# Kernel optimization log

Hardware: AMD Instinct MI355X
Metric: run time of the kernel (lower is better)

The kernel has to match this reference:

```python
import jax, jax.numpy as jnp
import numpy as np

B = 256      # number of drug pairs in the batch
N_PER = 40   # atoms per graph (equal-sized segments)
H = 128      # hidden_dim


def setup_inputs() -> dict:
    key = jax.random.key(0)
    k1, k2, kw1, kb1, kw2, kb2 = jax.random.split(key, 6)
    N = B * N_PER
    h1_atoms = jax.random.normal(k1, (N, H), dtype=jnp.float32)
    h2_atoms = jax.random.normal(k2, (N, H), dtype=jnp.float32)
    # sorted, equal-sized batch assignments (40 atoms per graph)
    batch1 = jnp.repeat(jnp.arange(B, dtype=jnp.int32), N_PER)
    batch2 = jnp.repeat(jnp.arange(B, dtype=jnp.int32), N_PER)
    s1 = 1.0 / np.sqrt(2 * H)
    s2 = 1.0 / np.sqrt(H)
    W1 = jax.random.uniform(kw1, (2 * H, H), jnp.float32, -s1, s1)
    b1 = jax.random.uniform(kb1, (H,), jnp.float32, -s1, s1)
    W2 = jax.random.uniform(kw2, (H, 1), jnp.float32, -s2, s2)
    b2 = jax.random.uniform(kb2, (1,), jnp.float32, -s2, s2)
    return {"h1_atoms": h1_atoms, "h2_atoms": h2_atoms, "batch1": batch1,
            "batch2": batch2, "W1": W1, "b1": b1, "W2": W2, "b2": b2}


def reference(h1_atoms, h2_atoms, batch1, batch2, W1, b1, W2, b2):
    # Equal-sized sorted segments -> reshape into [B, n, H] blocks.
    a1 = h1_atoms.reshape(B, N_PER, H)
    a2 = h2_atoms.reshape(B, N_PER, H)
    # cat([a1_exp, a2_exp], -1) @ W1  ==  a1 @ W1[:H] + a2 @ W1[H:]
    # (avoids materializing the [B,n1,n2,2H] concat)
    p1 = jnp.einsum('bid,dh->bih', a1, W1[:H])          # [B,n1,H]
    p2 = jnp.einsum('bjd,dh->bjh', a2, W1[H:])          # [B,n2,H]
    hidden = jnp.tanh(p1[:, :, None, :] + p2[:, None, :, :] + b1)  # [B,n1,n2,H]
    logits = jnp.einsum('bijh,h->bij', hidden, W2[:, 0]) + b2[0]   # [B,n1,n2]
    # global softmax over the flattened n1*n2 pair scores of each drug pair
    p = jax.nn.softmax(logits.reshape(B, -1), axis=-1).reshape(B, N_PER, N_PER)
    attn1 = p.sum(axis=2).reshape(-1)   # [num_atoms1]
    attn2 = p.sum(axis=1).reshape(-1)   # [num_atoms2]
    return attn1, attn2
```

## Files before the change

kernel.cpp:

```cpp
#include <hip/hip_runtime.h>

#define BB 256
#define NP 40
#define HH 128
#define EST 132
#define SST 44
#define NT 1024
#define AROWB 272
#define NROWP 48

typedef __attribute__((ext_vector_type(8))) short bf16x8;
typedef __attribute__((ext_vector_type(4))) float f32x4;

static __device__ __forceinline__ unsigned short f2bf(float f) {
    unsigned u = __float_as_uint(f);
    return (unsigned short)((u + 0x7FFFu + ((u >> 16) & 1u)) >> 16);
}

#define BATCH2(acc, ex0, ex1, ey0, ey1, ww0, ww1) do {            \
    float d0_ = fmaf((ex0), (ey0), 1.f);                          \
    float d1_ = fmaf((ex1), (ey1), 1.f);                          \
    float r_  = __builtin_amdgcn_rcpf(d0_ * d1_);                 \
    float n_  = fmaf((ww1), d0_, (ww0) * d1_);                    \
    acc = fmaf(n_, r_, acc);                                      \
} while (0)

__global__ __launch_bounds__(NT, 4) void ddi_fused(
    const float* __restrict__ h1, const float* __restrict__ h2,
    const float* __restrict__ W1, const float* __restrict__ b1,
    const float* __restrict__ W2, const float* __restrict__ b2,
    float* __restrict__ out)
{
    const int b = blockIdx.x;
    const int t = threadIdx.x;
    const int l = t & 63;
    const int w = t >> 6;

    __shared__ __align__(16) char  sAB[2*NROWP*AROWB];
    __shared__ __align__(16) float sE[2*NP*EST];
    __shared__ __align__(16) float sSE[NP*SST];
    __shared__ __align__(16) float sW2[HH];
    __shared__ float sRed[NT/64];
    __shared__ float sCL;

    const float L2E = 1.44269504088896340736f;
    const float K   = 2.88539008177792681472f;

    const int m  = w >> 3;
    const int hm = w & 7;
    const int hbase = hm*16 + ((l >> 4) << 2);
    const float* Wb = W1 + (size_t)m*HH*HH + hm*16 + (l & 15);
    float wraw[4][8];
    #pragma unroll
    for (int ks = 0; ks < 4; ++ks)
        #pragma unroll
        for (int j = 0; j < 8; ++j)
            wraw[ks][j] = Wb[(size_t)(ks*32 + ((l>>4)<<3) + j) * HH];
    float4 kbK = make_float4(0.f,0.f,0.f,0.f);
    if (m == 0) {
        float4 bv = *(const float4*)(b1 + hbase);
        kbK = make_float4(K*bv.x, K*bv.y, K*bv.z, K*bv.w);
    }

    #pragma unroll
    for (int pass = 0; pass < 2; ++pass) {
        int s = t + pass*NT;
        if (s < 2*NP*16) {
            int ms  = (s >= NP*16) ? 1 : 0;
            int rem = s - ms*NP*16;
            int r   = rem >> 4;
            int kg  = rem & 15;
            const float* src = (ms ? h2 : h1) + ((size_t)b*NP + r)*HH + kg*8;
            float4 v0 = *(const float4*)src;
            float4 v1 = *(const float4*)(src + 4);
            unsigned p0 = f2bf(v0.x) | ((unsigned)f2bf(v0.y) << 16);
            unsigned p1 = f2bf(v0.z) | ((unsigned)f2bf(v0.w) << 16);
            unsigned p2 = f2bf(v1.x) | ((unsigned)f2bf(v1.y) << 16);
            unsigned p3 = f2bf(v1.z) | ((unsigned)f2bf(v1.w) << 16);
            *(uint4*)(sAB + (ms*NROWP + r)*AROWB + kg*16) = make_uint4(p0,p1,p2,p3);
        }
    }
    if (t < HH) sW2[t] = W2[t];
    if (t < 64) {
        float c = W2[t] + W2[t + 64];
        #pragma unroll
        for (int off = 32; off > 0; off >>= 1) c += __shfl_down(c, off, 64);
        if (t == 0) sCL = (c + b2[0]) * L2E;
    }

    bf16x8 wf[4];
    #pragma unroll
    for (int ks = 0; ks < 4; ++ks) {
        #pragma unroll
        for (int j = 0; j < 8; ++j)
            ((unsigned short*)&wf[ks])[j] = f2bf(wraw[ks][j]);
    }
    __syncthreads();

    {
        const char* Ab = sAB + (m*NROWP + (l & 15))*AROWB + ((l >> 4) << 4);
        #pragma unroll
        for (int rn = 0; rn < 3; ++rn) {
            f32x4 c = {0.f, 0.f, 0.f, 0.f};
            #pragma unroll
            for (int ks = 0; ks < 4; ++ks) {
                bf16x8 af = *(const bf16x8*)(Ab + rn*(16*AROWB) + ks*64);
                c = __builtin_amdgcn_mfma_f32_16x16x32_bf16(wf[ks], af, c, 0, 0, 0);
            }
            int r = rn*16 + (l & 15);
            if (r < NP) {
                float4 ev;
                ev.x = __builtin_amdgcn_exp2f(fmaf(K, c[0], kbK.x));
                ev.y = __builtin_amdgcn_exp2f(fmaf(K, c[1], kbK.y));
                ev.z = __builtin_amdgcn_exp2f(fmaf(K, c[2], kbK.z));
                ev.w = __builtin_amdgcn_exp2f(fmaf(K, c[3], kbK.w));
                *(float4*)(sE + (m*NP + r)*EST + hbase) = ev;
            }
        }
    }
    __syncthreads();

    float lsum = 0.f;
    if (t < 800) {
        const int tile = t >> 2;
        const int hseg = t & 3;
        const int it = tile / 20;
        const int jt = tile - it * 20;
        const int h0 = hseg << 5;
        const float* e1b = sE + it*EST + h0;
        const float* e2b = sE + (NP + jt)*EST + h0;
        const float* wpb = sW2 + h0;
        float a[8];
        #pragma unroll
        for (int q = 0; q < 8; ++q) a[q] = 0.f;
        #pragma unroll
        for (int s = 0; s < 32; s += 4) {
            float4 wv = *(const float4*)(wpb + s);
            float4 e1v[4], e2v[2];
            #pragma unroll
            for (int rn = 0; rn < 4; ++rn) e1v[rn] = *(const float4*)(e1b + rn*10*EST + s);
            #pragma unroll
            for (int cn = 0; cn < 2; ++cn) e2v[cn] = *(const float4*)(e2b + cn*20*EST + s);
            #pragma unroll
            for (int rn = 0; rn < 4; ++rn)
                #pragma unroll
                for (int cn = 0; cn < 2; ++cn) {
                    BATCH2(a[rn*2+cn], e1v[rn].x, e1v[rn].y, e2v[cn].x, e2v[cn].y, wv.x, wv.y);
                    BATCH2(a[rn*2+cn], e1v[rn].z, e1v[rn].w, e2v[cn].z, e2v[cn].w, wv.z, wv.w);
                }
        }
        #pragma unroll
        for (int q = 0; q < 8; ++q) {
            a[q] += __shfl_xor(a[q], 1);
            a[q] += __shfl_xor(a[q], 2);
        }
        float s0 = (hseg==0) ? a[0] : (hseg==1) ? a[2] : (hseg==2) ? a[4] : a[6];
        float s1 = (hseg==0) ? a[1] : (hseg==1) ? a[3] : (hseg==2) ? a[5] : a[7];
        const float CL = sCL;
        const int row = it + 10*hseg;
        float pu0 = __builtin_amdgcn_exp2f(fmaf(s0, -K, CL));
        float pu1 = __builtin_amdgcn_exp2f(fmaf(s1, -K, CL));
        sSE[row*SST + jt]      = pu0;
        sSE[row*SST + jt + 20] = pu1;
        lsum = pu0 + pu1;
    }

    #pragma unroll
    for (int off = 32; off > 0; off >>= 1) lsum += __shfl_down(lsum, off, 64);
    if ((t & 63) == 0) sRed[t >> 6] = lsum;
    __syncthreads();
    float Z = 0.f;
    #pragma unroll
    for (int wv = 0; wv < NT/64; ++wv) Z += sRed[wv];
    const float rZ = __builtin_amdgcn_rcpf(Z);

    if (t < 320) {
        const int row = t >> 3, seg = t & 7;
        const float* p = sSE + row*SST + seg*5;
        float s = p[0] + p[1] + p[2] + p[3] + p[4];
        s += __shfl_down(s, 4, 8);
        s += __shfl_down(s, 2, 8);
        s += __shfl_down(s, 1, 8);
        if (seg == 0) out[b*NP + row] = s * rZ;
    } else if (t < 640) {
        const int q = t - 320;
        const int col = q >> 3, seg = q & 7;
        float s = 0.f;
        #pragma unroll
        for (int k = 0; k < 5; ++k) s += sSE[(seg*5 + k)*SST + col];
        s += __shfl_down(s, 4, 8);
        s += __shfl_down(s, 2, 8);
        s += __shfl_down(s, 1, 8);
        if (seg == 0) out[BB*NP + b*NP + col] = s * rZ;
    }
}

extern "C" void kernel_launch(void* const* d_in, const int* in_sizes, int n_in,
                              void* d_out, int out_size, void* d_ws, size_t ws_size,
                              hipStream_t stream) {
    const float* h1 = (const float*)d_in[0];
    const float* h2 = (const float*)d_in[1];
    const float* W1 = (const float*)d_in[4];
    const float* b1 = (const float*)d_in[5];
    const float* W2 = (const float*)d_in[6];
    const float* b2 = (const float*)d_in[7];
    float* out = (float*)d_out;

    hipLaunchKernelGGL(ddi_fused, dim3(BB), dim3(NT), 0, stream,
                       h1, h2, W1, b1, W2, b2, out);
}
```

Measured before the change: 17.48 us.

## Load atom rows straight into MFMA fragments with register double-buffering

Removes the shared-memory staging of bf16 atom features. Each lane now loads its own A-fragment rows from global memory, converts them to bf16 in registers and runs the MFMA directly, using two register buffers so the next row tile's load overlaps the current tile's compute and epilogue. This drops a __syncthreads and the LDS writes and reads, but each row is now loaded redundantly by all 8 hm waves instead of once. Register pressure also rises, and the launch_bounds occupancy hint of 4 is removed.

```diff
diff --git a/kernel.cpp b/kernel.cpp
--- a/kernel.cpp
+++ b/kernel.cpp
@@ -1,4 +1,5 @@
 #include <hip/hip_runtime.h>
+#include <hip/hip_bf16.h>
 
 #define BB 256
 #define NP 40
@@ -6,15 +7,14 @@
 #define EST 132
 #define SST 44
 #define NT 1024
-#define AROWB 272
-#define NROWP 48
 
 typedef __attribute__((ext_vector_type(8))) short bf16x8;
 typedef __attribute__((ext_vector_type(4))) float f32x4;
 
-static __device__ __forceinline__ unsigned short f2bf(float f) {
-    unsigned u = __float_as_uint(f);
-    return (unsigned short)((u + 0x7FFFu + ((u >> 16) & 1u)) >> 16);
+static __device__ __forceinline__ short bfs(float f) {
+    union { __hip_bfloat16 h; short s; } u;
+    u.h = __float2bfloat16(f);
+    return u.s;
 }
 
 #define BATCH2(acc, ex0, ex1, ey0, ey1, ww0, ww1) do {            \
@@ -25,7 +25,45 @@
     acc = fmaf(n_, r_, acc);                                      \
 } while (0)
 
-__global__ __launch_bounds__(NT, 4) void ddi_fused(
+#define LOADA(buf, rn) do {                                        \
+    int r_  = (rn)*16 + lr;                                        \
+    int rc_ = (r_ < NP) ? r_ : NP-1;    \
+    const float* s_ = Am + ((size_t)b*NP + rc_)*HH + (l4<<3);      \
+    _Pragma("unroll")                                              \
+    for (int ks_ = 0; ks_ < 4; ++ks_) {                            \
+        buf[2*ks_]   = *(const float4*)(s_ + ks_*32);              \
+        buf[2*ks_+1] = *(const float4*)(s_ + ks_*32 + 4);          \
+    }                                                              \
+} while (0)
+
+#define COMPUTE(buf, cacc) do {                                    \
+    bf16x8 af_[4];                                                 \
+    _Pragma("unroll")                                              \
+    for (int ks_ = 0; ks_ < 4; ++ks_) {                            \
+        short* ap_ = (short*)&af_[ks_];                            \
+        ap_[0]=bfs(buf[2*ks_].x);   ap_[1]=bfs(buf[2*ks_].y);      \
+        ap_[2]=bfs(buf[2*ks_].z);   ap_[3]=bfs(buf[2*ks_].w);      \
+        ap_[4]=bfs(buf[2*ks_+1].x); ap_[5]=bfs(buf[2*ks_+1].y);    \
+        ap_[6]=bfs(buf[2*ks_+1].z); ap_[7]=bfs(buf[2*ks_+1].w);    \
+    }                                                              \
+    _Pragma("unroll")                                              \
+    for (int ks_ = 0; ks_ < 4; ++ks_)                              \
+        cacc = __builtin_amdgcn_mfma_f32_16x16x32_bf16(wf[ks_], af_[ks_], cacc, 0, 0, 0); \
+} while (0)
+
+#define EPILOG(cacc, rn) do {                                      \
+    int r_ = (rn)*16 + lr;                                         \
+    if (r_ < NP) {                                                 \
+        float4 ev_;                                                \
+        ev_.x = __builtin_amdgcn_exp2f(fmaf(K, cacc[0], kbK.x));   \
+        ev_.y = __builtin_amdgcn_exp2f(fmaf(K, cacc[1], kbK.y));   \
+        ev_.z = __builtin_amdgcn_exp2f(fmaf(K, cacc[2], kbK.z));   \
+        ev_.w = __builtin_amdgcn_exp2f(fmaf(K, cacc[3], kbK.w));   \
+        *(float4*)(sE + (m*NP + r_)*EST + hbase) = ev_;            \
+    }                                                              \
+} while (0)
+
+__global__ __launch_bounds__(NT) void ddi_fused(
     const float* __restrict__ h1, const float* __restrict__ h2,
     const float* __restrict__ W1, const float* __restrict__ b1,
     const float* __restrict__ W2, const float* __restrict__ b2,
@@ -36,7 +74,6 @@
     const int l = t & 63;
     const int w = t >> 6;
 
-    __shared__ __align__(16) char  sAB[2*NROWP*AROWB];
     __shared__ __align__(16) float sE[2*NP*EST];
     __shared__ __align__(16) float sSE[NP*SST];
     __shared__ __align__(16) float sW2[HH];
@@ -48,38 +85,27 @@
 
     const int m  = w >> 3;
     const int hm = w & 7;
-    const int hbase = hm*16 + ((l >> 4) << 2);
-    const float* Wb = W1 + (size_t)m*HH*HH + hm*16 + (l & 15);
+    const int l4 = l >> 4;
+    const int lr = l & 15;
+    const int hbase = hm*16 + l4*4;
+    const float* Am = m ? h2 : h1;
+
+    const float* Wb = W1 + (size_t)m*HH*HH + hm*16 + lr;
     float wraw[4][8];
     #pragma unroll
     for (int ks = 0; ks < 4; ++ks)
         #pragma unroll
         for (int j = 0; j < 8; ++j)
-            wraw[ks][j] = Wb[(size_t)(ks*32 + ((l>>4)<<3) + j) * HH];
+            wraw[ks][j] = Wb[(size_t)(ks*32 + (l4<<3) + j) * HH];
+
+    float4 aA[8], aB[8];
+    LOADA(aA, 0);
+
     float4 kbK = make_float4(0.f,0.f,0.f,0.f);
     if (m == 0) {
         float4 bv = *(const float4*)(b1 + hbase);
         kbK = make_float4(K*bv.x, K*bv.y, K*bv.z, K*bv.w);
     }
-
-    #pragma unroll
-    for (int pass = 0; pass < 2; ++pass) {
-        int s = t + pass*NT;
-        if (s < 2*NP*16) {
-            int ms  = (s >= NP*16) ? 1 : 0;
-            int rem = s - ms*NP*16;
-            int r   = rem >> 4;
-            int kg  = rem & 15;
-            const float* src = (ms ? h2 : h1) + ((size_t)b*NP + r)*HH + kg*8;
-            float4 v0 = *(const float4*)src;
-            float4 v1 = *(const float4*)(src + 4);
-            unsigned p0 = f2bf(v0.x) | ((unsigned)f2bf(v0.y) << 16);
-            unsigned p1 = f2bf(v0.z) | ((unsigned)f2bf(v0.w) << 16);
-            unsigned p2 = f2bf(v1.x) | ((unsigned)f2bf(v1.y) << 16);
-            unsigned p3 = f2bf(v1.z) | ((unsigned)f2bf(v1.w) << 16);
-            *(uint4*)(sAB + (ms*NROWP + r)*AROWB + kg*16) = make_uint4(p0,p1,p2,p3);
-        }
-    }
     if (t < HH) sW2[t] = W2[t];
     if (t < 64) {
         float c = W2[t] + W2[t + 64];
@@ -91,33 +117,21 @@
     bf16x8 wf[4];
     #pragma unroll
     for (int ks = 0; ks < 4; ++ks) {
-        #pragma unroll
-        for (int j = 0; j < 8; ++j)
-            ((unsigned short*)&wf[ks])[j] = f2bf(wraw[ks][j]);
-    }
-    __syncthreads();
-
-    {
-        const char* Ab = sAB + (m*NROWP + (l & 15))*AROWB + ((l >> 4) << 4);
-        #pragma unroll
-        for (int rn = 0; rn < 3; ++rn) {
-            f32x4 c = {0.f, 0.f, 0.f, 0.f};
-            #pragma unroll
-            for (int ks = 0; ks < 4; ++ks) {
-                bf16x8 af = *(const bf16x8*)(Ab + rn*(16*AROWB) + ks*64);
-                c = __builtin_amdgcn_mfma_f32_16x16x32_bf16(wf[ks], af, c, 0, 0, 0);
-            }
-            int r = rn*16 + (l & 15);
-            if (r < NP) {
-                float4 ev;
-                ev.x = __builtin_amdgcn_exp2f(fmaf(K, c[0], kbK.x));
-                ev.y = __builtin_amdgcn_exp2f(fmaf(K, c[1], kbK.y));
-                ev.z = __builtin_amdgcn_exp2f(fmaf(K, c[2], kbK.z));
-                ev.w = __builtin_amdgcn_exp2f(fmaf(K, c[3], kbK.w));
-                *(float4*)(sE + (m*NP + r)*EST + hbase) = ev;
-            }
-        }
-    }
+        short* wp = (short*)&wf[ks];
+        #pragma unroll
+        for (int j = 0; j < 8; ++j) wp[j] = bfs(wraw[ks][j]);
+    }
+
+    f32x4 c0 = {0.f,0.f,0.f,0.f}, c1 = c0, c2 = c0;
+    COMPUTE(aA, c0);
+    LOADA(aB, 1);
+    EPILOG(c0, 0);
+    COMPUTE(aB, c1);
+    LOADA(aA, 2);
+    EPILOG(c1, 1);
+    COMPUTE(aA, c2);
+    EPILOG(c2, 2);
+
     __syncthreads();
 
     float lsum = 0.f;
```

Measured after the change: 24.73 us. +41.4%, slower.

## Split each drug pair across two half-row blocks with a second normalization kernel

Applied to the files above, without the earlier changes.

Each drug pair is now handled by two 512-thread blocks, each covering 20 of the 40 rows of the first graph. Partial softmax sums and row/column sums go to a workspace, and a small second kernel combines them and normalizes. The aim is to double the grid size and shrink each block for better occupancy and load balance across CUs. In exchange, each block recomputes the full h2 projection (redundant MFMA work), an extra kernel launch is added, and results make a round trip through global memory.

```diff
diff --git a/kernel.cpp b/kernel.cpp
--- a/kernel.cpp
+++ b/kernel.cpp
@@ -1,20 +1,22 @@
 #include <hip/hip_runtime.h>
+#include <hip/hip_bf16.h>
 
 #define BB 256
 #define NP 40
 #define HH 128
 #define EST 132
 #define SST 44
-#define NT 1024
+#define NT1 512
 #define AROWB 272
-#define NROWP 48
+#define WSPP 128
 
 typedef __attribute__((ext_vector_type(8))) short bf16x8;
 typedef __attribute__((ext_vector_type(4))) float f32x4;
 
-static __device__ __forceinline__ unsigned short f2bf(float f) {
-    unsigned u = __float_as_uint(f);
-    return (unsigned short)((u + 0x7FFFu + ((u >> 16) & 1u)) >> 16);
+static __device__ __forceinline__ short bfs(float f) {
+    union { __hip_bfloat16 h; short s; } u;
+    u.h = __float2bfloat16(f);
+    return u.s;
 }
 
 #define BATCH2(acc, ex0, ex1, ey0, ey1, ww0, ww1) do {            \
@@ -25,59 +27,57 @@
     acc = fmaf(n_, r_, acc);                                      \
 } while (0)
 
-__global__ __launch_bounds__(NT, 4) void ddi_fused(
+__global__ __launch_bounds__(NT1, 4) void ddi_k1(
     const float* __restrict__ h1, const float* __restrict__ h2,
     const float* __restrict__ W1, const float* __restrict__ b1,
     const float* __restrict__ W2, const float* __restrict__ b2,
-    float* __restrict__ out)
+    float* __restrict__ ws)
 {
-    const int b = blockIdx.x;
+    const int b    = blockIdx.x >> 1;
+    const int half = blockIdx.x & 1;
     const int t = threadIdx.x;
     const int l = t & 63;
     const int w = t >> 6;
-
-    __shared__ __align__(16) char  sAB[2*NROWP*AROWB];
-    __shared__ __align__(16) float sE[2*NP*EST];
-    __shared__ __align__(16) float sSE[NP*SST];
+    const int l4 = l >> 4;
+    const int lr = l & 15;
+    const int hm = w;
+    const int hbase = hm*16 + l4*4;
+
+    __shared__ __align__(16) char  sAB[60*AROWB];
+    __shared__ __align__(16) float sE[60*EST];
+    __shared__ __align__(16) float sSE[20*SST];
     __shared__ __align__(16) float sW2[HH];
-    __shared__ float sRed[NT/64];
+    __shared__ float sRed[8];
     __shared__ float sCL;
 
     const float L2E = 1.44269504088896340736f;
     const float K   = 2.88539008177792681472f;
 
-    const int m  = w >> 3;
-    const int hm = w & 7;
-    const int hbase = hm*16 + ((l >> 4) << 2);
-    const float* Wb = W1 + (size_t)m*HH*HH + hm*16 + (l & 15);
+    const float* Wb0 = W1 + hm*16 + lr;
+    const float* Wb1 = W1 + (size_t)HH*HH + hm*16 + lr;
     float wraw[4][8];
     #pragma unroll
     for (int ks = 0; ks < 4; ++ks)
         #pragma unroll
         for (int j = 0; j < 8; ++j)
-            wraw[ks][j] = Wb[(size_t)(ks*32 + ((l>>4)<<3) + j) * HH];
-    float4 kbK = make_float4(0.f,0.f,0.f,0.f);
-    if (m == 0) {
-        float4 bv = *(const float4*)(b1 + hbase);
-        kbK = make_float4(K*bv.x, K*bv.y, K*bv.z, K*bv.w);
-    }
+            wraw[ks][j] = Wb0[(size_t)(ks*32 + (l4<<3) + j) * HH];
 
     #pragma unroll
     for (int pass = 0; pass < 2; ++pass) {
-        int s = t + pass*NT;
-        if (s < 2*NP*16) {
-            int ms  = (s >= NP*16) ? 1 : 0;
-            int rem = s - ms*NP*16;
-            int r   = rem >> 4;
-            int kg  = rem & 15;
-            const float* src = (ms ? h2 : h1) + ((size_t)b*NP + r)*HH + kg*8;
+        int s = t + pass*NT1;
+        if (s < 60*16) {
+            int r  = s >> 4;
+            int kg = s & 15;
+            const float* src = (r < 20)
+                ? h1 + ((size_t)b*NP + half*20 + r)*HH + kg*8
+                : h2 + ((size_t)b*NP + (r-20))*HH + kg*8;
             float4 v0 = *(const float4*)src;
             float4 v1 = *(const float4*)(src + 4);
-            unsigned p0 = f2bf(v0.x) | ((unsigned)f2bf(v0.y) << 16);
-            unsigned p1 = f2bf(v0.z) | ((unsigned)f2bf(v0.w) << 16);
-            unsigned p2 = f2bf(v1.x) | ((unsigned)f2bf(v1.y) << 16);
-            unsigned p3 = f2bf(v1.z) | ((unsigned)f2bf(v1.w) << 16);
-            *(uint4*)(sAB + (ms*NROWP + r)*AROWB + kg*16) = make_uint4(p0,p1,p2,p3);
+            unsigned p0 = (unsigned short)bfs(v0.x) | ((unsigned)(unsigned short)bfs(v0.y) << 16);
+            unsigned p1 = (unsigned short)bfs(v0.z) | ((unsigned)(unsigned short)bfs(v0.w) << 16);
+            unsigned p2 = (unsigned short)bfs(v1.x) | ((unsigned)(unsigned short)bfs(v1.y) << 16);
+            unsigned p3 = (unsigned short)bfs(v1.z) | ((unsigned)(unsigned short)bfs(v1.w) << 16);
+            *(uint4*)(sAB + r*AROWB + kg*16) = make_uint4(p0,p1,p2,p3);
         }
     }
     if (t < HH) sW2[t] = W2[t];
@@ -88,47 +88,82 @@
         if (t == 0) sCL = (c + b2[0]) * L2E;
     }
 
-    bf16x8 wf[4];
+    bf16x8 wf0[4], wf1[4];
     #pragma unroll
     for (int ks = 0; ks < 4; ++ks) {
+        short* wp = (short*)&wf0[ks];
+        #pragma unroll
+        for (int j = 0; j < 8; ++j) wp[j] = bfs(wraw[ks][j]);
+    }
+    #pragma unroll
+    for (int ks = 0; ks < 4; ++ks)
         #pragma unroll
         for (int j = 0; j < 8; ++j)
-            ((unsigned short*)&wf[ks])[j] = f2bf(wraw[ks][j]);
+            wraw[ks][j] = Wb1[(size_t)(ks*32 + (l4<<3) + j) * HH];
+    #pragma unroll
+    for (int ks = 0; ks < 4; ++ks) {
+        short* wp = (short*)&wf1[ks];
+        #pragma unroll
+        for (int j = 0; j < 8; ++j) wp[j] = bfs(wraw[ks][j]);
+    }
+    float4 kbK;
+    {
+        float4 bv = *(const float4*)(b1 + hbase);
+        kbK = make_float4(K*bv.x, K*bv.y, K*bv.z, K*bv.w);
     }
     __syncthreads();
 
-    {
-        const char* Ab = sAB + (m*NROWP + (l & 15))*AROWB + ((l >> 4) << 4);
-        #pragma unroll
-        for (int rn = 0; rn < 3; ++rn) {
-            f32x4 c = {0.f, 0.f, 0.f, 0.f};
-            #pragma unroll
-            for (int ks = 0; ks < 4; ++ks) {
-                bf16x8 af = *(const bf16x8*)(Ab + rn*(16*AROWB) + ks*64);
-                c = __builtin_amdgcn_mfma_f32_16x16x32_bf16(wf[ks], af, c, 0, 0, 0);
-            }
-            int r = rn*16 + (l & 15);
-            if (r < NP) {
-                float4 ev;
-                ev.x = __builtin_amdgcn_exp2f(fmaf(K, c[0], kbK.x));
-                ev.y = __builtin_amdgcn_exp2f(fmaf(K, c[1], kbK.y));
-                ev.z = __builtin_amdgcn_exp2f(fmaf(K, c[2], kbK.z));
-                ev.w = __builtin_amdgcn_exp2f(fmaf(K, c[3], kbK.w));
-                *(float4*)(sE + (m*NP + r)*EST + hbase) = ev;
-            }
+    #pragma unroll
+    for (int rn = 0; rn < 2; ++rn) {
+        int rr = rn*16 + lr;
+        int rowc = (rr < 20) ? rr : 19;
+        const char* Ab = sAB + rowc*AROWB + (l4 << 4);
+        f32x4 c = {0.f,0.f,0.f,0.f};
+        #pragma unroll
+        for (int ks = 0; ks < 4; ++ks) {
+            bf16x8 af = *(const bf16x8*)(Ab + ks*64);
+            c = __builtin_amdgcn_mfma_f32_16x16x32_bf16(wf0[ks], af, c, 0, 0, 0);
+        }
+        if (rr < 20) {
+            float4 ev;
+            ev.x = __builtin_amdgcn_exp2f(fmaf(K, c[0], kbK.x));
+            ev.y = __builtin_amdgcn_exp2f(fmaf(K, c[1], kbK.y));
+            ev.z = __builtin_amdgcn_exp2f(fmaf(K, c[2], kbK.z));
+            ev.w = __builtin_amdgcn_exp2f(fmaf(K, c[3], kbK.w));
+            *(float4*)(sE + rr*EST + hbase) = ev;
+        }
+    }
+    #pragma unroll
+    for (int rn = 0; rn < 3; ++rn) {
+        int rr = rn*16 + lr;
+        int rowc = (rr < 40) ? rr : 39;
+        const char* Ab = sAB + (20 + rowc)*AROWB + (l4 << 4);
+        f32x4 c = {0.f,0.f,0.f,0.f};
+        #pragma unroll
+        for (int ks = 0; ks < 4; ++ks) {
+            bf16x8 af = *(const bf16x8*)(Ab + ks*64);
+            c = __builtin_amdgcn_mfma_f32_16x16x32_bf16(wf1[ks], af, c, 0, 0, 0);
+        }
+        if (rr < 40) {
+            float4 ev;
+            ev.x = __builtin_amdgcn_exp2f(K * c[0]);
+            ev.y = __builtin_amdgcn_exp2f(K * c[1]);
+            ev.z = __builtin_amdgcn_exp2f(K * c[2]);
+            ev.w = __builtin_amdgcn_exp2f(K * c[3]);
+            *(float4*)(sE + (20 + rr)*EST + hbase) = ev;
         }
     }
     __syncthreads();
 
     float lsum = 0.f;
-    if (t < 800) {
+    if (t < 400) {
         const int tile = t >> 2;
         const int hseg = t & 3;
         const int it = tile / 20;
-        const int jt = tile - it * 20;
+        const int jt = tile - it*20;
         const int h0 = hseg << 5;
         const float* e1b = sE + it*EST + h0;
-        const float* e2b = sE + (NP + jt)*EST + h0;
+        const float* e2b = sE + (20 + jt)*EST + h0;
         const float* wpb = sW2 + h0;
         float a[8];
         #pragma unroll
@@ -138,7 +173,7 @@
             float4 wv = *(const float4*)(wpb + s);
             float4 e1v[4], e2v[2];
             #pragma unroll
-            for (int rn = 0; rn < 4; ++rn) e1v[rn] = *(const float4*)(e1b + rn*10*EST + s);
+            for (int rn = 0; rn < 4; ++rn) e1v[rn] = *(const float4*)(e1b + rn*5*EST + s);
             #pragma unroll
             for (int cn = 0; cn < 2; ++cn) e2v[cn] = *(const float4*)(e2b + cn*20*EST + s);
             #pragma unroll
@@ -157,7 +192,7 @@
         float s0 = (hseg==0) ? a[0] : (hseg==1) ? a[2] : (hseg==2) ? a[4] : a[6];
         float s1 = (hseg==0) ? a[1] : (hseg==1) ? a[3] : (hseg==2) ? a[5] : a[7];
         const float CL = sCL;
-        const int row = it + 10*hseg;
+        const int row = it + 5*hseg;
         float pu0 = __builtin_amdgcn_exp2f(fmaf(s0, -K, CL));
         float pu1 = __builtin_amdgcn_exp2f(fmaf(s1, -K, CL));
         sSE[row*SST + jt]      = pu0;
@@ -171,27 +206,42 @@
     __syncthreads();
     float Z = 0.f;
     #pragma unroll
-    for (int wv = 0; wv < NT/64; ++wv) Z += sRed[wv];
-    const float rZ = __builtin_amdgcn_rcpf(Z);
-
-    if (t < 320) {
+    for (int wv = 0; wv < 8; ++wv) Z += sRed[wv];
+
+    float* wsp = ws + (size_t)b*WSPP + half*64;
+    if (t == 0) wsp[0] = Z;
+    if (t < 160) {
         const int row = t >> 3, seg = t & 7;
         const float* p = sSE + row*SST + seg*5;
         float s = p[0] + p[1] + p[2] + p[3] + p[4];
         s += __shfl_down(s, 4, 8);
         s += __shfl_down(s, 2, 8);
         s += __shfl_down(s, 1, 8);
-        if (seg == 0) out[b*NP + row] = s * rZ;
-    } else if (t < 640) {
-        const int q = t - 320;
-        const int col = q >> 3, seg = q & 7;
+        if (seg == 0) wsp[1 + row] = s;
+    } else if (t >= 192 && t < 352) {
+        const int q = t - 192;
+        const int col = q >> 2, seg = q & 3;
         float s = 0.f;
         #pragma unroll
         for (int k = 0; k < 5; ++k) s += sSE[(seg*5 + k)*SST + col];
-        s += __shfl_down(s, 4, 8);
-        s += __shfl_down(s, 2, 8);
-        s += __shfl_down(s, 1, 8);
-        if (seg == 0) out[BB*NP + b*NP + col] = s * rZ;
+        s += __shfl_down(s, 2, 4);
+        s += __shfl_down(s, 1, 4);
+        if (seg == 0) wsp[21 + col] = s;
+    }
+}
+
+__global__ __launch_bounds__(64) void ddi_k2(const float* __restrict__ ws,
+                                            float* __restrict__ out)
+{
+    const int b = blockIdx.x;
+    const int t = threadIdx.x;
+    const float* base = ws + (size_t)b*WSPP;
+    const float Z = base[0] + base[64];
+    const float rZ = 1.0f / Z;
+    if (t < 40) {
+        float r1 = (t < 20) ? base[1 + t] : base[45 + t];
+        out[b*NP + t] = r1 * rZ;
+        out[BB*NP + b*NP + t] = (base[21 + t] + base[85 + t]) * rZ;
     }
 }
 
@@ -205,7 +255,9 @@
     const float* W2 = (const float*)d_in[6];
     const float* b2 = (const float*)d_in[7];
     float* out = (float*)d_out;
-
-    hipLaunchKernelGGL(ddi_fused, dim3(BB), dim3(NT), 0, stream,
-                       h1, h2, W1, b1, W2, b2, out);
-}
+    float* ws  = (float*)d_ws;
+
+    hipLaunchKernelGGL(ddi_k1, dim3(2*BB), dim3(NT1), 0, stream,
+                       h1, h2, W1, b1, W2, b2, ws);
+    hipLaunchKernelGGL(ddi_k2, dim3(BB), dim3(64), 0, stream, ws, out);
+}
```

After: 20.61 us. 1.18x slower.
